# Kernel tuning notes

Measured on AMD Instinct MI355X. Metric: run time of the kernel, lower is better.

Reference implementation:

```python
import math
import jax, jax.numpy as jnp
import numpy as np

B, L = 64, 25
FEAT, HEADS, LAYERS = 128, 8, 2
USER_N, POI_N, CAT_N = 5000, 10000, 400


def _autocorr(q, k, v):
    # q,k,v: [B,L,H,E] ; training-mode AutoCorrelation (self.training=True)
    Lq = q.shape[1]
    qp = jnp.transpose(q, (0, 2, 3, 1))  # [B,H,E,L]
    kp = jnp.transpose(k, (0, 2, 3, 1))
    vp = jnp.transpose(v, (0, 2, 3, 1))
    qf = jnp.fft.rfft(qp, axis=-1)
    kf = jnp.fft.rfft(kp, axis=-1)
    corr = jnp.fft.irfft(qf * jnp.conj(kf), n=Lq, axis=-1)  # [B,H,E,L]
    top_k = int(1 * math.log(Lq))  # factor=1 -> 3 for L=25
    mean_value = corr.mean(axis=(1, 2))  # [B,L]
    _, index = jax.lax.top_k(mean_value.mean(axis=0), top_k)  # [K], shared across batch
    weights = mean_value[:, index]  # [B,K]
    tmp_corr = jax.nn.softmax(weights, axis=-1)
    # roll(values, -delay) == gather at (t + delay) mod L
    gidx = (jnp.arange(Lq)[None, :] + index[:, None]) % Lq  # [K,L]
    patterns = vp[..., gidx]  # [B,H,E,K,L]
    agg = jnp.einsum('bhekl,bk->bhel', patterns, tmp_corr)  # weighted delay aggregation
    return jnp.transpose(agg, (0, 3, 1, 2))  # [B,L,H,E]


def _ac_layer(qx, kx, vx, w, b):
    # w: [4, d, d] torch-layout [out,in] for (q,k,v,out) projections; b: [4, d]
    Bq, Lq, d = qx.shape
    q = (qx @ w[0].T + b[0]).reshape(Bq, Lq, HEADS, -1)
    k = (kx @ w[1].T + b[1]).reshape(Bq, kx.shape[1], HEADS, -1)
    v = (vx @ w[2].T + b[2]).reshape(Bq, vx.shape[1], HEADS, -1)
    out = _autocorr(q, k, v).reshape(Bq, Lq, -1)
    return out @ w[3].T + b[3]


def setup_inputs() -> dict:
    key = jax.random.key(0)
    ks = jax.random.split(key, 16)
    d = FEAT
    inp = {
        'user': jax.random.randint(ks[0], (B, L), 0, USER_N),
        'poi': jax.random.randint(ks[1], (B, L), 0, POI_N),
        'cat': jax.random.randint(ks[2], (B, L), 0, CAT_N),
        'lat': jax.random.normal(ks[3], (B, L), jnp.float32),
        'lon': jax.random.normal(ks[4], (B, L), jnp.float32),
        'tod': jax.random.randint(ks[5], (B, L), 0, 24),
        'dow': jax.random.randint(ks[6], (B, L), 0, 7),
        'unixtime': jax.random.normal(ks[7], (B, L), jnp.float32),
        'user_emb': jax.random.normal(ks[8], (USER_N, d), jnp.float32) * 0.02,
        'poi_emb': jax.random.normal(ks[9], (POI_N, d), jnp.float32) * 0.02,
        'cat_emb': jax.random.normal(ks[10], (CAT_N, d), jnp.float32) * 0.02,
        'tod_emb': jax.random.normal(ks[11], (24, d), jnp.float32) * 0.02,
        'dow_emb': jax.random.normal(ks[12], (7, d), jnp.float32) * 0.02,
        'user_embc': jax.random.normal(jax.random.fold_in(ks[8], 1), (USER_N, d), jnp.float32) * 0.02,
        'tod_embc': jax.random.normal(jax.random.fold_in(ks[11], 1), (24, d), jnp.float32) * 0.02,
        'dow_embc': jax.random.normal(jax.random.fold_in(ks[12], 1), (7, d), jnp.float32) * 0.02,
        # W[layer, module(poi,cat,xpoi,xcat), proj(q,k,v,o), out, in]
        'W': jax.random.normal(ks[13], (LAYERS, 4, 4, d, d), jnp.float32) * (1.0 / math.sqrt(d)),
        'Bv': jnp.zeros((LAYERS, 4, 4, d), jnp.float32),
        'value_w': jax.random.normal(ks[14], (1, L), jnp.float32) * 0.1,
        'value_b': jnp.zeros((1,), jnp.float32),
        'distance_matrix': jax.random.uniform(ks[15], (POI_N, POI_N), jnp.float32) * 10.0,
    }
    return inp


def reference(user, poi, cat, lat, lon, tod, dow, unixtime,
              user_emb, poi_emb, cat_emb, tod_emb, dow_emb,
              user_embc, tod_embc, dow_embc,
              W, Bv, value_w, value_b, distance_matrix):
    x = user_emb[user] + poi_emb[poi] + tod_emb[tod] + dow_emb[dow]        # [B,L,d]
    xc = user_embc[user] + cat_emb[cat] + tod_embc[tod] + dow_embc[dow]   # [B,L,d]

    interval_dis = distance_matrix[poi]  # [B,L,P] row gather == index_select loop
    interval = jnp.exp(-interval_dis / (interval_dis.max() - interval_dis.min()))

    out, outc = x, xc
    for i in range(LAYERS):
        out = _ac_layer(out, out, out, W[i, 0], Bv[i, 0])
        outc = _ac_layer(outc, outc, outc, W[i, 1], Bv[i, 1])
        out = _ac_layer(out, outc, outc, W[i, 2], Bv[i, 2])
        outc = _ac_layer(outc, out, out, W[i, 3], Bv[i, 3])

    attn = jnp.einsum('pd,bld->bpl', poi_emb, out) * jnp.transpose(interval, (0, 2, 1))
    attn_cat = jnp.einsum('cd,bld->bcl', cat_emb, outc)
    pre_poi = (attn @ value_w.T + value_b)[..., 0]      # [B,P]
    pre_cat = (attn_cat @ value_w.T + value_b)[..., 0]  # [B,C]
    return pre_poi, pre_cat
```

## Files before the change

kernel.cpp:

```cpp
#include <hip/hip_runtime.h>
#include <hip/hip_bf16.h>

#define BB 64
#define LL 25
#define DD 128
#define BL 1600
#define POI_N 10000
#define CAT_N 400

__global__ __launch_bounds__(256) void embed_kernel(
    const int* __restrict__ user, const int* __restrict__ poi, const int* __restrict__ cat,
    const int* __restrict__ tod, const int* __restrict__ dow,
    const float* __restrict__ ue, const float* __restrict__ pe, const float* __restrict__ ce,
    const float* __restrict__ te, const float* __restrict__ de,
    const float* __restrict__ uec, const float* __restrict__ tec, const float* __restrict__ dec,
    float* __restrict__ x, float* __restrict__ xc, unsigned* __restrict__ mm)
{
    int idx = blockIdx.x * 256 + threadIdx.x;
    if (idx == 0) { mm[0] = 0u; mm[1] = 0x7f7fffffu; }
    int bl = idx >> 7, d = idx & 127;
    int u = user[bl], p = poi[bl], c = cat[bl], td = tod[bl], dw = dow[bl];
    x[idx]  = ue[u * DD + d] + pe[p * DD + d] + te[td * DD + d] + de[dw * DD + d];
    xc[idx] = uec[u * DD + d] + ce[c * DD + d] + tec[td * DD + d] + dec[dw * DD + d];
}

__global__ __launch_bounds__(256) void minmax_kernel(
    const int* __restrict__ poi, const float* __restrict__ Dm, unsigned* __restrict__ mm)
{
    int bl = blockIdx.x;
    const float4* r = (const float4*)(Dm + (size_t)poi[bl] * POI_N);
    float mx = -1e30f, mn = 1e30f;
    for (int i = threadIdx.x; i < POI_N / 4; i += 256) {
        float4 v4 = r[i];
        mx = fmaxf(mx, fmaxf(fmaxf(v4.x, v4.y), fmaxf(v4.z, v4.w)));
        mn = fminf(mn, fminf(fminf(v4.x, v4.y), fminf(v4.z, v4.w)));
    }
    for (int off = 32; off > 0; off >>= 1) {
        mx = fmaxf(mx, __shfl_down(mx, off));
        mn = fminf(mn, __shfl_down(mn, off));
    }
    __shared__ float smx[4], smn[4];
    int lid = threadIdx.x & 63, wid = threadIdx.x >> 6;
    if (lid == 0) { smx[wid] = mx; smn[wid] = mn; }
    __syncthreads();
    if (threadIdx.x == 0) {
        mx = fmaxf(fmaxf(smx[0], smx[1]), fmaxf(smx[2], smx[3]));
        mn = fminf(fminf(smn[0], smn[1]), fminf(smn[2], smn[3]));
        atomicMax(&mm[0], __float_as_uint(mx));
        atomicMin(&mm[1], __float_as_uint(mn));
    }
}

__global__ __launch_bounds__(256) void proj_kernel(
    const float* __restrict__ sq, const float* __restrict__ sk, const float* __restrict__ sv,
    const float* __restrict__ Wbase, const float* __restrict__ Bbase,
    float* __restrict__ q, float* __restrict__ k, float* __restrict__ v)
{
    int r = blockIdx.y;
    const float* src = (r == 0) ? sq : (r == 1 ? sk : sv);
    float* dst       = (r == 0) ? q  : (r == 1 ? k  : v);
    const float* Wm   = Wbase + r * DD * DD;
    const float* bias = Bbase + r * DD;
    int mbase = blockIdx.x * 32;
    __shared__ float sS[32][132];
    __shared__ float sWc[128][68];
    int t = threadIdx.x;

    for (int i = t; i < 32 * 32; i += 256) {
        int m = i >> 5, c = (i & 31) << 2;
        *(float4*)&sS[m][c] = *(const float4*)(src + (mbase + m) * DD + c);
    }
    __syncthreads();

    int nh = t & 31, mg = t >> 5;
    float acc[4][4] = {};
    for (int kb = 0; kb < 128; kb += 64) {
        for (int i = t; i < 128 * 16; i += 256) {
            int n = i >> 4, c = (i & 15) << 2;
            *(float4*)&sWc[n][c] = *(const float4*)(Wm + n * DD + kb + c);
        }
        __syncthreads();
#pragma unroll 4
        for (int kk = 0; kk < 64; kk += 4) {
            float4 a[4], w[4];
#pragma unroll
            for (int i2 = 0; i2 < 4; i2++) a[i2] = *(const float4*)&sS[mg * 4 + i2][kb + kk];
#pragma unroll
            for (int j = 0; j < 4; j++) w[j] = *(const float4*)&sWc[nh + 32 * j][kk];
#pragma unroll
            for (int i2 = 0; i2 < 4; i2++)
#pragma unroll
                for (int j = 0; j < 4; j++)
                    acc[i2][j] += a[i2].x * w[j].x + a[i2].y * w[j].y +
                                  a[i2].z * w[j].z + a[i2].w * w[j].w;
        }
        __syncthreads();
    }
#pragma unroll
    for (int i2 = 0; i2 < 4; i2++) {
        int m = mbase + mg * 4 + i2;
#pragma unroll
        for (int j = 0; j < 4; j++) {
            int n = nh + 32 * j;
            dst[m * DD + n] = acc[i2][j] + bias[n];
        }
    }
}

__global__ __launch_bounds__(256) void corr_kernel(
    const float* __restrict__ q, const float* __restrict__ k, float* __restrict__ mv)
{
    int b = blockIdx.x;
    __shared__ float sq[LL * DD], sk[LL * DD];
    __shared__ float rbuf[LL][4];
    int t = threadIdx.x;
    for (int i = t; i < 800; i += 256) {
        int c = i << 2;
        *(float4*)&sq[c] = *(const float4*)(q + b * LL * DD + c);
        *(float4*)&sk[c] = *(const float4*)(k + b * LL * DD + c);
    }
    __syncthreads();
    int lid = t & 63, wid = t >> 6;
    for (int tau = 0; tau < LL; tau++) {
        float s = 0.f;
        for (int e = t; e < LL * DD; e += 256) {
            int srow = e >> 7, d = e & 127;
            int qrow = srow + tau; if (qrow >= LL) qrow -= LL;
            s += sq[qrow * DD + d] * sk[e];
        }
        for (int off = 32; off > 0; off >>= 1) s += __shfl_down(s, off);
        if (lid == 0) rbuf[tau][wid] = s;
    }
    __syncthreads();
    if (t < LL)
        mv[b * LL + t] = (rbuf[t][0] + rbuf[t][1] + rbuf[t][2] + rbuf[t][3]) * (1.0f / 128.0f);
}

__global__ void topsm_kernel(const float* __restrict__ mv, float* __restrict__ tc,
                             int* __restrict__ idxout)
{
    __shared__ float sbm[LL];
    __shared__ int sidx[3];
    int t = threadIdx.x;
    if (t < LL) {
        float s = 0.f;
        for (int b = 0; b < BB; b++) s += mv[b * LL + t];
        sbm[t] = s;
    }
    __syncthreads();
    if (t == 0) {
        float loc[LL];
        for (int i = 0; i < LL; i++) loc[i] = sbm[i];
        for (int j = 0; j < 3; j++) {
            int bi = 0; float bvv = loc[0];
            for (int i = 1; i < LL; i++) if (loc[i] > bvv) { bvv = loc[i]; bi = i; }
            sidx[j] = bi; idxout[j] = bi; loc[bi] = -1e30f;
        }
    }
    __syncthreads();
    if (t < BB) {
        float w0 = mv[t * LL + sidx[0]];
        float w1 = mv[t * LL + sidx[1]];
        float w2 = mv[t * LL + sidx[2]];
        float m = fmaxf(w0, fmaxf(w1, w2));
        float e0 = expf(w0 - m), e1 = expf(w1 - m), e2 = expf(w2 - m);
        float inv = 1.0f / (e0 + e1 + e2);
        tc[t * 4 + 0] = e0 * inv; tc[t * 4 + 1] = e1 * inv; tc[t * 4 + 2] = e2 * inv;
    }
}

__global__ __launch_bounds__(256) void aggproj_kernel(
    const float* __restrict__ v, const float* __restrict__ tc, const int* __restrict__ idx3,
    const float* __restrict__ Wm, const float* __restrict__ bias, float* __restrict__ dst)
{
    int mbase = blockIdx.x * 32;
    __shared__ float sS[32][132];
    __shared__ float sWc[128][68];
    int t = threadIdx.x;
    int i0 = idx3[0], i1 = idx3[1], i2x = idx3[2];

    for (int i = t; i < 32 * 32; i += 256) {
        int m = i >> 5, c = (i & 31) << 2;
        int row = mbase + m;
        int b = row / LL, l = row - b * LL;
        int l0 = l + i0;  if (l0 >= LL) l0 -= LL;
        int l1 = l + i1;  if (l1 >= LL) l1 -= LL;
        int l2 = l + i2x; if (l2 >= LL) l2 -= LL;
        float w0 = tc[b * 4 + 0], w1 = tc[b * 4 + 1], w2 = tc[b * 4 + 2];
        float4 v0 = *(const float4*)(v + (b * LL + l0) * DD + c);
        float4 v1 = *(const float4*)(v + (b * LL + l1) * DD + c);
        float4 v2 = *(const float4*)(v + (b * LL + l2) * DD + c);
        float4 a;
        a.x = w0 * v0.x + w1 * v1.x + w2 * v2.x;
        a.y = w0 * v0.y + w1 * v1.y + w2 * v2.y;
        a.z = w0 * v0.z + w1 * v1.z + w2 * v2.z;
        a.w = w0 * v0.w + w1 * v1.w + w2 * v2.w;
        *(float4*)&sS[m][c] = a;
    }
    __syncthreads();

    int nh = t & 31, mg = t >> 5;
    float acc[4][4] = {};
    for (int kb = 0; kb < 128; kb += 64) {
        for (int i = t; i < 128 * 16; i += 256) {
            int n = i >> 4, c = (i & 15) << 2;
            *(float4*)&sWc[n][c] = *(const float4*)(Wm + n * DD + kb + c);
        }
        __syncthreads();
#pragma unroll 4
        for (int kk = 0; kk < 64; kk += 4) {
            float4 a[4], w[4];
#pragma unroll
            for (int ii = 0; ii < 4; ii++) a[ii] = *(const float4*)&sS[mg * 4 + ii][kb + kk];
#pragma unroll
            for (int j = 0; j < 4; j++) w[j] = *(const float4*)&sWc[nh + 32 * j][kk];
#pragma unroll
            for (int ii = 0; ii < 4; ii++)
#pragma unroll
                for (int j = 0; j < 4; j++)
                    acc[ii][j] += a[ii].x * w[j].x + a[ii].y * w[j].y +
                                  a[ii].z * w[j].z + a[ii].w * w[j].w;
        }
        __syncthreads();
    }
#pragma unroll
    for (int ii = 0; ii < 4; ii++) {
        int m = mbase + mg * 4 + ii;
#pragma unroll
        for (int j = 0; j < 4; j++) {
            int n = nh + 32 * j;
            dst[m * DD + n] = acc[ii][j] + bias[n];
        }
    }
}

__global__ __launch_bounds__(256) void precat_kernel(
    const float* __restrict__ outc, const float* __restrict__ cat_emb,
    const float* __restrict__ vw, const float* __restrict__ vbp, float* __restrict__ dstc)
{
    int b = blockIdx.x, t = threadIdx.x;
    __shared__ float y[DD];
    __shared__ float svw[LL];
    if (t < LL) svw[t] = vw[t];
    __syncthreads();
    if (t < DD) {
        float s = 0.f;
        for (int l = 0; l < LL; l++) s += svw[l] * outc[(b * LL + l) * DD + t];
        y[t] = s;
    }
    __syncthreads();
    float vb = vbp[0];
    for (int c = t; c < CAT_N; c += 256) {
        float s = 0.f;
        for (int d = 0; d < DD; d += 4) {
            float4 ce4 = *(const float4*)(cat_emb + c * DD + d);
            s += ce4.x * y[d] + ce4.y * y[d + 1] + ce4.z * y[d + 2] + ce4.w * y[d + 3];
        }
        dstc[b * CAT_N + c] = s + vb;
    }
}

__global__ __launch_bounds__(256) void prepoi_kernel(
    const float* __restrict__ outp, const float* __restrict__ poi_emb,
    const int* __restrict__ poi_idx, const float* __restrict__ Dm,
    const unsigned* __restrict__ mm, const float* __restrict__ vw,
    const float* __restrict__ vbp, float* __restrict__ dstp)
{
    int b = blockIdx.y;
    int pbase = blockIdx.x << 7;
    __shared__ float sO[LL][132];
    __shared__ float sPc[128][68];
    __shared__ float sS[LL][132];
    __shared__ float svw[LL];
    __shared__ int srow[LL];
    __shared__ float red[128];
    int t = threadIdx.x;

    for (int i = t; i < 800; i += 256) {
        int l = i >> 5, c = (i & 31) << 2;
        *(float4*)&sO[l][c] = *(const float4*)(outp + (b * LL + l) * DD + c);
    }
    if (t < LL) { svw[t] = vw[t]; srow[t] = poi_idx[b * LL + t]; }
    __syncthreads();

    int nh = t & 31, mg = t >> 5;
    float acc[4][4] = {};
    for (int kb = 0; kb < 128; kb += 64) {
        for (int i = t; i < 128 * 16; i += 256) {
            int p = i >> 4, c = (i & 15) << 2;
            float4 val = {0.f, 0.f, 0.f, 0.f};
            if (pbase + p < POI_N) val = *(const float4*)(poi_emb + (pbase + p) * DD + kb + c);
            *(float4*)&sPc[p][c] = val;
        }
        __syncthreads();
#pragma unroll 4
        for (int kk = 0; kk < 64; kk += 4) {
            float4 a0 = *(const float4*)&sO[mg][kb + kk];
            float4 a1 = *(const float4*)&sO[mg + 8][kb + kk];
            float4 a2 = *(const float4*)&sO[mg + 16][kb + kk];
            float4 a3 = {0.f, 0.f, 0.f, 0.f};
            if (mg == 0) a3 = *(const float4*)&sO[24][kb + kk];
#pragma unroll
            for (int j = 0; j < 4; j++) {
                float4 p4 = *(const float4*)&sPc[nh + 32 * j][kk];
                acc[j][0] += p4.x * a0.x + p4.y * a0.y + p4.z * a0.z + p4.w * a0.w;
                acc[j][1] += p4.x * a1.x + p4.y * a1.y + p4.z * a1.z + p4.w * a1.w;
                acc[j][2] += p4.x * a2.x + p4.y * a2.y + p4.z * a2.z + p4.w * a2.w;
                acc[j][3] += p4.x * a3.x + p4.y * a3.y + p4.z * a3.z + p4.w * a3.w;
            }
        }
        __syncthreads();
    }
#pragma unroll
    for (int j = 0; j < 4; j++) {
        int pl = nh + 32 * j;
        sS[mg][pl]      = acc[j][0];
        sS[mg + 8][pl]  = acc[j][1];
        sS[mg + 16][pl] = acc[j][2];
        if (mg == 0) sS[24][pl] = acc[j][3];
    }
    __syncthreads();

    float gmax = __uint_as_float(mm[0]);
    float gmin = __uint_as_float(mm[1]);
    float ninv = -1.0f / (gmax - gmin);
    int pp = t & 127, half = t >> 7;
    int p = pbase + pp;
    float s = 0.f;
    if (p < POI_N) {
        int l0 = half ? 13 : 0, l1 = half ? 25 : 13;
        for (int l = l0; l < l1; l++) {
            float dv = Dm[(size_t)srow[l] * POI_N + p];
            s += svw[l] * expf(dv * ninv) * sS[l][pp];
        }
    }
    if (half) red[pp] = s;
    __syncthreads();
    if (!half && p < POI_N)
        dstp[(size_t)b * POI_N + p] = s + red[pp] + vbp[0];
}

extern "C" void kernel_launch(void* const* d_in, const int* in_sizes, int n_in,
                              void* d_out, int out_size, void* d_ws, size_t ws_size,
                              hipStream_t stream)
{
    const int*   user = (const int*)d_in[0];
    const int*   poi  = (const int*)d_in[1];
    const int*   cat  = (const int*)d_in[2];
    const int*   tod  = (const int*)d_in[5];
    const int*   dow  = (const int*)d_in[6];
    const float* ue   = (const float*)d_in[8];
    const float* pe   = (const float*)d_in[9];
    const float* ce   = (const float*)d_in[10];
    const float* te   = (const float*)d_in[11];
    const float* de   = (const float*)d_in[12];
    const float* uec  = (const float*)d_in[13];
    const float* tec  = (const float*)d_in[14];
    const float* dec  = (const float*)d_in[15];
    const float* W    = (const float*)d_in[16];
    const float* Bv   = (const float*)d_in[17];
    const float* vw   = (const float*)d_in[18];
    const float* vb   = (const float*)d_in[19];
    const float* Dm   = (const float*)d_in[20];

    float* ws = (float*)d_ws;
    float* O0 = ws;
    float* C0 = ws + 204800;
    float* O1 = ws + 409600;
    float* C1 = ws + 614400;
    float* Q  = ws + 819200;
    float* Kb = ws + 1024000;
    float* V  = ws + 1228800;
    float* MV = ws + 1433600;
    float* TC = ws + 1435200;
    int*   IDX = (int*)(ws + 1435456);
    unsigned* MM = (unsigned*)(ws + 1435460);

    float* out_poi = (float*)d_out;
    float* out_cat = out_poi + BB * POI_N;

    embed_kernel<<<800, 256, 0, stream>>>(user, poi, cat, tod, dow,
                                          ue, pe, ce, te, de, uec, tec, dec, O0, C0, MM);
    minmax_kernel<<<BL, 256, 0, stream>>>(poi, Dm, MM);

    auto ac = [&](const float* qx, const float* kx, const float* vx, int i, int j, float* dstbuf) {
        const float* Wb = W + (size_t)((i * 4 + j) * 4) * DD * DD;
        const float* Bb = Bv + (size_t)((i * 4 + j) * 4) * DD;
        proj_kernel<<<dim3(50, 3), 256, 0, stream>>>(qx, kx, vx, Wb, Bb, Q, Kb, V);
        corr_kernel<<<BB, 256, 0, stream>>>(Q, Kb, MV);
        topsm_kernel<<<1, 256, 0, stream>>>(MV, TC, IDX);
        aggproj_kernel<<<50, 256, 0, stream>>>(V, TC, IDX, Wb + 3 * DD * DD, Bb + 3 * DD, dstbuf);
    };

    ac(O0, O0, O0, 0, 0, O1);
    ac(C0, C0, C0, 0, 1, C1);
    ac(O1, C1, C1, 0, 2, O0);
    ac(C1, O0, O0, 0, 3, C0);
    ac(O0, O0, O0, 1, 0, O1);
    ac(C0, C0, C0, 1, 1, C1);
    ac(O1, C1, C1, 1, 2, O0);
    ac(C1, O0, O0, 1, 3, C0);

    precat_kernel<<<BB, 256, 0, stream>>>(C0, ce, vw, vb, out_cat);
    prepoi_kernel<<<dim3(79, BB), 256, 0, stream>>>(O0, pe, poi, Dm, MM, vw, vb, out_poi);
}
```

Before: 1.203 ms.

## Fuse embed, minmax, and all autocorrelation layers into one persistent kernel with grid barriers

Replaces the embed, minmax, and 32 per-layer kernel launches (projection, correlation, top-k/softmax, aggregation+projection) plus precat with a single persistent kernel of 150 blocks that synchronizes stages through atomic-counter grid barriers. Top-k/softmax is recomputed redundantly in each aggregation block instead of running as a separate single-block kernel. The min is tracked with atomicMax on the bitwise complement so a single memset can zero both counters. This removes launch overhead and inter-kernel gaps, but relies on all 150 blocks being co-resident for the spin barriers and loses the extra parallelism from splitting minmax over 1600 blocks.

```diff
diff --git a/kernel.cpp b/kernel.cpp
--- a/kernel.cpp
+++ b/kernel.cpp
@@ -1,5 +1,4 @@
 #include <hip/hip_runtime.h>
-#include <hip/hip_bf16.h>
 
 #define BB 64
 #define LL 25
@@ -7,256 +6,293 @@
 #define BL 1600
 #define POI_N 10000
 #define CAT_N 400
-
-__global__ __launch_bounds__(256) void embed_kernel(
+#define NBLK 150
+
+__device__ __forceinline__ void gridbar(unsigned* __restrict__ bar, int id)
+{
+    __syncthreads();
+    if (threadIdx.x == 0) {
+        __threadfence();
+        __hip_atomic_fetch_add(&bar[id], 1u, __ATOMIC_RELEASE, __HIP_MEMORY_SCOPE_AGENT);
+        while (__hip_atomic_load(&bar[id], __ATOMIC_ACQUIRE, __HIP_MEMORY_SCOPE_AGENT) < NBLK)
+            __builtin_amdgcn_s_sleep(1);
+    }
+    __syncthreads();
+}
+
+__global__ __launch_bounds__(256) void persist_kernel(
     const int* __restrict__ user, const int* __restrict__ poi, const int* __restrict__ cat,
     const int* __restrict__ tod, const int* __restrict__ dow,
     const float* __restrict__ ue, const float* __restrict__ pe, const float* __restrict__ ce,
     const float* __restrict__ te, const float* __restrict__ de,
     const float* __restrict__ uec, const float* __restrict__ tec, const float* __restrict__ dec,
-    float* __restrict__ x, float* __restrict__ xc, unsigned* __restrict__ mm)
+    const float* __restrict__ W, const float* __restrict__ Bv,
+    const float* __restrict__ vw, const float* __restrict__ vbp,
+    const float* __restrict__ Dm,
+    float* __restrict__ O0, float* __restrict__ C0, float* __restrict__ O1, float* __restrict__ C1,
+    float* __restrict__ Qb, float* __restrict__ Kb, float* __restrict__ Vb,
+    float* __restrict__ MV,
+    unsigned* __restrict__ bar, unsigned* __restrict__ mm,
+    float* __restrict__ out_cat)
 {
-    int idx = blockIdx.x * 256 + threadIdx.x;
-    if (idx == 0) { mm[0] = 0u; mm[1] = 0x7f7fffffu; }
-    int bl = idx >> 7, d = idx & 127;
-    int u = user[bl], p = poi[bl], c = cat[bl], td = tod[bl], dw = dow[bl];
-    x[idx]  = ue[u * DD + d] + pe[p * DD + d] + te[td * DD + d] + de[dw * DD + d];
-    xc[idx] = uec[u * DD + d] + ce[c * DD + d] + tec[td * DD + d] + dec[dw * DD + d];
-}
-
-__global__ __launch_bounds__(256) void minmax_kernel(
-    const int* __restrict__ poi, const float* __restrict__ Dm, unsigned* __restrict__ mm)
-{
-    int bl = blockIdx.x;
-    const float4* r = (const float4*)(Dm + (size_t)poi[bl] * POI_N);
-    float mx = -1e30f, mn = 1e30f;
-    for (int i = threadIdx.x; i < POI_N / 4; i += 256) {
-        float4 v4 = r[i];
-        mx = fmaxf(mx, fmaxf(fmaxf(v4.x, v4.y), fmaxf(v4.z, v4.w)));
-        mn = fminf(mn, fminf(fminf(v4.x, v4.y), fminf(v4.z, v4.w)));
-    }
-    for (int off = 32; off > 0; off >>= 1) {
-        mx = fmaxf(mx, __shfl_down(mx, off));
-        mn = fminf(mn, __shfl_down(mn, off));
-    }
-    __shared__ float smx[4], smn[4];
-    int lid = threadIdx.x & 63, wid = threadIdx.x >> 6;
-    if (lid == 0) { smx[wid] = mx; smn[wid] = mn; }
-    __syncthreads();
-    if (threadIdx.x == 0) {
-        mx = fmaxf(fmaxf(smx[0], smx[1]), fmaxf(smx[2], smx[3]));
-        mn = fminf(fminf(smn[0], smn[1]), fminf(smn[2], smn[3]));
-        atomicMax(&mm[0], __float_as_uint(mx));
-        atomicMin(&mm[1], __float_as_uint(mn));
-    }
-}
-
-__global__ __launch_bounds__(256) void proj_kernel(
-    const float* __restrict__ sq, const float* __restrict__ sk, const float* __restrict__ sv,
-    const float* __restrict__ Wbase, const float* __restrict__ Bbase,
-    float* __restrict__ q, float* __restrict__ k, float* __restrict__ v)
-{
-    int r = blockIdx.y;
-    const float* src = (r == 0) ? sq : (r == 1 ? sk : sv);
-    float* dst       = (r == 0) ? q  : (r == 1 ? k  : v);
-    const float* Wm   = Wbase + r * DD * DD;
-    const float* bias = Bbase + r * DD;
-    int mbase = blockIdx.x * 32;
-    __shared__ float sS[32][132];
-    __shared__ float sWc[128][68];
-    int t = threadIdx.x;
-
-    for (int i = t; i < 32 * 32; i += 256) {
-        int m = i >> 5, c = (i & 31) << 2;
-        *(float4*)&sS[m][c] = *(const float4*)(src + (mbase + m) * DD + c);
-    }
-    __syncthreads();
-
-    int nh = t & 31, mg = t >> 5;
-    float acc[4][4] = {};
-    for (int kb = 0; kb < 128; kb += 64) {
-        for (int i = t; i < 128 * 16; i += 256) {
-            int n = i >> 4, c = (i & 15) << 2;
-            *(float4*)&sWc[n][c] = *(const float4*)(Wm + n * DD + kb + c);
-        }
+    __shared__ __align__(16) char smem_raw[51712];
+    float (*sS)[132] = reinterpret_cast<float(*)[132]>(smem_raw);
+    float (*sWc)[68] = reinterpret_cast<float(*)[68]>(smem_raw + 16896);
+    float* csq       = reinterpret_cast<float*>(smem_raw);
+    float* csk       = reinterpret_cast<float*>(smem_raw + 12800);
+    float (*crb)[4]  = reinterpret_cast<float(*)[4]>(smem_raw + 25600);
+
+    __shared__ float sbm[LL];
+    __shared__ int   sidx[3];
+    __shared__ float stc[BB][3];
+    __shared__ float redA[4], redB[4];
+    __shared__ float yv[DD];
+    __shared__ float svw[LL];
+
+    int bx = blockIdx.x, t = threadIdx.x;
+
+    for (int i = bx * 256 + t; i < 51200; i += NBLK * 256) {
+        int bl = i >> 5, c = (i & 31) << 2;
+        int u = user[bl], p = poi[bl], cc = cat[bl], td = tod[bl], dw = dow[bl];
+        float4 a0 = *(const float4*)(ue + u * DD + c);
+        float4 a1 = *(const float4*)(pe + p * DD + c);
+        float4 a2 = *(const float4*)(te + td * DD + c);
+        float4 a3 = *(const float4*)(de + dw * DD + c);
+        float4 x;
+        x.x = a0.x + a1.x + a2.x + a3.x; x.y = a0.y + a1.y + a2.y + a3.y;
+        x.z = a0.z + a1.z + a2.z + a3.z; x.w = a0.w + a1.w + a2.w + a3.w;
+        *(float4*)(O0 + bl * DD + c) = x;
+        float4 b0 = *(const float4*)(uec + u * DD + c);
+        float4 b1 = *(const float4*)(ce + cc * DD + c);
+        float4 b2 = *(const float4*)(tec + td * DD + c);
+        float4 b3 = *(const float4*)(dec + dw * DD + c);
+        float4 xc;
+        xc.x = b0.x + b1.x + b2.x + b3.x; xc.y = b0.y + b1.y + b2.y + b3.y;
+        xc.z = b0.z + b1.z + b2.z + b3.z; xc.w = b0.w + b1.w + b2.w + b3.w;
+        *(float4*)(C0 + bl * DD + c) = xc;
+    }
+    {
+        float mx = -1e30f, mn = 1e30f;
+        for (int row = bx; row < BL; row += NBLK) {
+            const float4* r4 = (const float4*)(Dm + (size_t)poi[row] * POI_N);
+            for (int i = t; i < POI_N / 4; i += 256) {
+                float4 v4 = r4[i];
+                mx = fmaxf(mx, fmaxf(fmaxf(v4.x, v4.y), fmaxf(v4.z, v4.w)));
+                mn = fminf(mn, fminf(fminf(v4.x, v4.y), fminf(v4.z, v4.w)));
+            }
+        }
+        for (int off = 32; off > 0; off >>= 1) {
+            mx = fmaxf(mx, __shfl_down(mx, off));
+            mn = fminf(mn, __shfl_down(mn, off));
+        }
+        if ((t & 63) == 0) { redA[t >> 6] = mx; redB[t >> 6] = mn; }
         __syncthreads();
+        if (t == 0) {
+            mx = fmaxf(fmaxf(redA[0], redA[1]), fmaxf(redA[2], redA[3]));
+            mn = fminf(fminf(redB[0], redB[1]), fminf(redB[2], redB[3]));
+            atomicMax(&mm[0], __float_as_uint(mx));
+            atomicMax(&mm[1], ~__float_as_uint(mn));
+        }
+    }
+    gridbar(bar, 0);
+
+    float* bufs[4] = {O0, C0, O1, C1};
+    const int qsel[8] = {0, 1, 2, 3, 0, 1, 2, 3};
+    const int ksel[8] = {0, 1, 3, 0, 0, 1, 3, 0};
+    const int dsel[8] = {2, 3, 0, 1, 2, 3, 0, 1};
+    int bid = 1;
+
+#pragma unroll 1
+    for (int ci = 0; ci < 8; ++ci) {
+        const float* qx  = bufs[qsel[ci]];
+        const float* kx  = bufs[ksel[ci]];
+        float*       dst = bufs[dsel[ci]];
+        const float* Wb  = W  + (size_t)ci * 4 * DD * DD;
+        const float* Bb  = Bv + (size_t)ci * 4 * DD;
+
+        {
+            int r = bx / 50, tile = bx % 50;
+            const float* src  = (r == 0) ? qx : kx;
+            const float* Wm   = Wb + r * DD * DD;
+            const float* bias = Bb + r * DD;
+            float* pdst       = (r == 0) ? Qb : (r == 1 ? Kb : Vb);
+            int mbase = tile * 32;
+
+            for (int i = t; i < 32 * 32; i += 256) {
+                int m = i >> 5, c = (i & 31) << 2;
+                *(float4*)&sS[m][c] = *(const float4*)(src + (mbase + m) * DD + c);
+            }
+            __syncthreads();
+            int nh = t & 31, mg = t >> 5;
+            float acc[4][4] = {};
+            for (int kb = 0; kb < 128; kb += 64) {
+                for (int i = t; i < 128 * 16; i += 256) {
+                    int n = i >> 4, c = (i & 15) << 2;
+                    *(float4*)&sWc[n][c] = *(const float4*)(Wm + n * DD + kb + c);
+                }
+                __syncthreads();
 #pragma unroll 4
-        for (int kk = 0; kk < 64; kk += 4) {
-            float4 a[4], w[4];
-#pragma unroll
-            for (int i2 = 0; i2 < 4; i2++) a[i2] = *(const float4*)&sS[mg * 4 + i2][kb + kk];
-#pragma unroll
-            for (int j = 0; j < 4; j++) w[j] = *(const float4*)&sWc[nh + 32 * j][kk];
-#pragma unroll
-            for (int i2 = 0; i2 < 4; i2++)
-#pragma unroll
-                for (int j = 0; j < 4; j++)
-                    acc[i2][j] += a[i2].x * w[j].x + a[i2].y * w[j].y +
-                                  a[i2].z * w[j].z + a[i2].w * w[j].w;
-        }
+                for (int kk = 0; kk < 64; kk += 4) {
+                    float4 a[4], w[4];
+#pragma unroll
+                    for (int i2 = 0; i2 < 4; i2++) a[i2] = *(const float4*)&sS[mg * 4 + i2][kb + kk];
+#pragma unroll
+                    for (int j = 0; j < 4; j++) w[j] = *(const float4*)&sWc[nh + 32 * j][kk];
+#pragma unroll
+                    for (int i2 = 0; i2 < 4; i2++)
+#pragma unroll
+                        for (int j = 0; j < 4; j++)
+                            acc[i2][j] += a[i2].x * w[j].x + a[i2].y * w[j].y +
+                                          a[i2].z * w[j].z + a[i2].w * w[j].w;
+                }
+                __syncthreads();
+            }
+#pragma unroll
+            for (int i2 = 0; i2 < 4; i2++) {
+                int m = mbase + mg * 4 + i2;
+#pragma unroll
+                for (int j = 0; j < 4; j++) {
+                    int n = nh + 32 * j;
+                    pdst[m * DD + n] = acc[i2][j] + bias[n];
+                }
+            }
+        }
+        gridbar(bar, bid++);
+
+        if (bx < BB) {
+            int b = bx;
+            for (int i = t; i < 800; i += 256) {
+                int c = i << 2;
+                *(float4*)&csq[c] = *(const float4*)(Qb + b * LL * DD + c);
+                *(float4*)&csk[c] = *(const float4*)(Kb + b * LL * DD + c);
+            }
+            __syncthreads();
+            int lid = t & 63, wid = t >> 6;
+            for (int tau = 0; tau < LL; tau++) {
+                float s = 0.f;
+                for (int e = t; e < 800; e += 256) {
+                    int srow = e >> 5, dc = (e & 31) << 2;
+                    int qrow = srow + tau; if (qrow >= LL) qrow -= LL;
+                    float4 a = *(const float4*)&csq[qrow * DD + dc];
+                    float4 g = *(const float4*)&csk[srow * DD + dc];
+                    s += a.x * g.x + a.y * g.y + a.z * g.z + a.w * g.w;
+                }
+                for (int off = 32; off > 0; off >>= 1) s += __shfl_down(s, off);
+                if (lid == 0) crb[tau][wid] = s;
+            }
+            __syncthreads();
+            if (t < LL)
+                MV[b * LL + t] = (crb[t][0] + crb[t][1] + crb[t][2] + crb[t][3]) * (1.0f / 128.0f);
+        }
+        gridbar(bar, bid++);
+
+        if (bx < 50) {
+            int mbase = bx * 32;
+            if (t < LL) {
+                float s = 0.f;
+                for (int b2 = 0; b2 < BB; b2++) s += MV[b2 * LL + t];
+                sbm[t] = s;
+            }
+            __syncthreads();
+            if (t == 0) {
+                float loc[LL];
+                for (int i = 0; i < LL; i++) loc[i] = sbm[i];
+                for (int j = 0; j < 3; j++) {
+                    int bi = 0; float bvv = loc[0];
+                    for (int i = 1; i < LL; i++) if (loc[i] > bvv) { bvv = loc[i]; bi = i; }
+                    sidx[j] = bi; loc[bi] = -1e30f;
+                }
+            }
+            __syncthreads();
+            if (t < BB) {
+                float w0 = MV[t * LL + sidx[0]];
+                float w1 = MV[t * LL + sidx[1]];
+                float w2 = MV[t * LL + sidx[2]];
+                float m = fmaxf(w0, fmaxf(w1, w2));
+                float e0 = expf(w0 - m), e1 = expf(w1 - m), e2 = expf(w2 - m);
+                float inv = 1.0f / (e0 + e1 + e2);
+                stc[t][0] = e0 * inv; stc[t][1] = e1 * inv; stc[t][2] = e2 * inv;
+            }
+            __syncthreads();
+            int i0 = sidx[0], i1 = sidx[1], i2x = sidx[2];
+            const float* Wm   = Wb + 3 * DD * DD;
+            const float* bias = Bb + 3 * DD;
+
+            for (int i = t; i < 32 * 32; i += 256) {
+                int m = i >> 5, c = (i & 31) << 2;
+                int row = mbase + m;
+                int b = row / LL, l = row - b * LL;
+                int l0 = l + i0;  if (l0 >= LL) l0 -= LL;
+                int l1 = l + i1;  if (l1 >= LL) l1 -= LL;
+                int l2 = l + i2x; if (l2 >= LL) l2 -= LL;
+                float w0 = stc[b][0], w1 = stc[b][1], w2 = stc[b][2];
+                float4 v0 = *(const float4*)(Vb + (b * LL + l0) * DD + c);
+                float4 v1 = *(const float4*)(Vb + (b * LL + l1) * DD + c);
+                float4 v2 = *(const float4*)(Vb + (b * LL + l2) * DD + c);
+                float4 a;
+                a.x = w0 * v0.x + w1 * v1.x + w2 * v2.x;
+                a.y = w0 * v0.y + w1 * v1.y + w2 * v2.y;
+                a.z = w0 * v0.z + w1 * v1.z + w2 * v2.z;
+                a.w = w0 * v0.w + w1 * v1.w + w2 * v2.w;
+                *(float4*)&sS[m][c] = a;
+            }
+            __syncthreads();
+            int nh = t & 31, mg = t >> 5;
+            float acc[4][4] = {};
+            for (int kb = 0; kb < 128; kb += 64) {
+                for (int i = t; i < 128 * 16; i += 256) {
+                    int n = i >> 4, c = (i & 15) << 2;
+                    *(float4*)&sWc[n][c] = *(const float4*)(Wm + n * DD + kb + c);
+                }
+                __syncthreads();
+#pragma unroll 4
+                for (int kk = 0; kk < 64; kk += 4) {
+                    float4 a[4], w[4];
+#pragma unroll
+                    for (int ii = 0; ii < 4; ii++) a[ii] = *(const float4*)&sS[mg * 4 + ii][kb + kk];
+#pragma unroll
+                    for (int j = 0; j < 4; j++) w[j] = *(const float4*)&sWc[nh + 32 * j][kk];
+#pragma unroll
+                    for (int ii = 0; ii < 4; ii++)
+#pragma unroll
+                        for (int j = 0; j < 4; j++)
+                            acc[ii][j] += a[ii].x * w[j].x + a[ii].y * w[j].y +
+                                          a[ii].z * w[j].z + a[ii].w * w[j].w;
+                }
+                __syncthreads();
+            }
+#pragma unroll
+            for (int ii = 0; ii < 4; ii++) {
+                int m = mbase + mg * 4 + ii;
+#pragma unroll
+                for (int j = 0; j < 4; j++) {
+                    int n = nh + 32 * j;
+                    dst[m * DD + n] = acc[ii][j] + bias[n];
+                }
+            }
+        }
+        gridbar(bar, bid++);
+    }
+
+    if (bx < BB) {
+        int b = bx;
+        if (t < LL) svw[t] = vw[t];
         __syncthreads();
-    }
-#pragma unroll
-    for (int i2 = 0; i2 < 4; i2++) {
-        int m = mbase + mg * 4 + i2;
-#pragma unroll
-        for (int j = 0; j < 4; j++) {
-            int n = nh + 32 * j;
-            dst[m * DD + n] = acc[i2][j] + bias[n];
-        }
-    }
-}
-
-__global__ __launch_bounds__(256) void corr_kernel(
-    const float* __restrict__ q, const float* __restrict__ k, float* __restrict__ mv)
-{
-    int b = blockIdx.x;
-    __shared__ float sq[LL * DD], sk[LL * DD];
-    __shared__ float rbuf[LL][4];
-    int t = threadIdx.x;
-    for (int i = t; i < 800; i += 256) {
-        int c = i << 2;
-        *(float4*)&sq[c] = *(const float4*)(q + b * LL * DD + c);
-        *(float4*)&sk[c] = *(const float4*)(k + b * LL * DD + c);
-    }
-    __syncthreads();
-    int lid = t & 63, wid = t >> 6;
-    for (int tau = 0; tau < LL; tau++) {
-        float s = 0.f;
-        for (int e = t; e < LL * DD; e += 256) {
-            int srow = e >> 7, d = e & 127;
-            int qrow = srow + tau; if (qrow >= LL) qrow -= LL;
-            s += sq[qrow * DD + d] * sk[e];
-        }
-        for (int off = 32; off > 0; off >>= 1) s += __shfl_down(s, off);
-        if (lid == 0) rbuf[tau][wid] = s;
-    }
-    __syncthreads();
-    if (t < LL)
-        mv[b * LL + t] = (rbuf[t][0] + rbuf[t][1] + rbuf[t][2] + rbuf[t][3]) * (1.0f / 128.0f);
-}
-
-__global__ void topsm_kernel(const float* __restrict__ mv, float* __restrict__ tc,
-                             int* __restrict__ idxout)
-{
-    __shared__ float sbm[LL];
-    __shared__ int sidx[3];
-    int t = threadIdx.x;
-    if (t < LL) {
-        float s = 0.f;
-        for (int b = 0; b < BB; b++) s += mv[b * LL + t];
-        sbm[t] = s;
-    }
-    __syncthreads();
-    if (t == 0) {
-        float loc[LL];
-        for (int i = 0; i < LL; i++) loc[i] = sbm[i];
-        for (int j = 0; j < 3; j++) {
-            int bi = 0; float bvv = loc[0];
-            for (int i = 1; i < LL; i++) if (loc[i] > bvv) { bvv = loc[i]; bi = i; }
-            sidx[j] = bi; idxout[j] = bi; loc[bi] = -1e30f;
-        }
-    }
-    __syncthreads();
-    if (t < BB) {
-        float w0 = mv[t * LL + sidx[0]];
-        float w1 = mv[t * LL + sidx[1]];
-        float w2 = mv[t * LL + sidx[2]];
-        float m = fmaxf(w0, fmaxf(w1, w2));
-        float e0 = expf(w0 - m), e1 = expf(w1 - m), e2 = expf(w2 - m);
-        float inv = 1.0f / (e0 + e1 + e2);
-        tc[t * 4 + 0] = e0 * inv; tc[t * 4 + 1] = e1 * inv; tc[t * 4 + 2] = e2 * inv;
-    }
-}
-
-__global__ __launch_bounds__(256) void aggproj_kernel(
-    const float* __restrict__ v, const float* __restrict__ tc, const int* __restrict__ idx3,
-    const float* __restrict__ Wm, const float* __restrict__ bias, float* __restrict__ dst)
-{
-    int mbase = blockIdx.x * 32;
-    __shared__ float sS[32][132];
-    __shared__ float sWc[128][68];
-    int t = threadIdx.x;
-    int i0 = idx3[0], i1 = idx3[1], i2x = idx3[2];
-
-    for (int i = t; i < 32 * 32; i += 256) {
-        int m = i >> 5, c = (i & 31) << 2;
-        int row = mbase + m;
-        int b = row / LL, l = row - b * LL;
-        int l0 = l + i0;  if (l0 >= LL) l0 -= LL;
-        int l1 = l + i1;  if (l1 >= LL) l1 -= LL;
-        int l2 = l + i2x; if (l2 >= LL) l2 -= LL;
-        float w0 = tc[b * 4 + 0], w1 = tc[b * 4 + 1], w2 = tc[b * 4 + 2];
-        float4 v0 = *(const float4*)(v + (b * LL + l0) * DD + c);
-        float4 v1 = *(const float4*)(v + (b * LL + l1) * DD + c);
-        float4 v2 = *(const float4*)(v + (b * LL + l2) * DD + c);
-        float4 a;
-        a.x = w0 * v0.x + w1 * v1.x + w2 * v2.x;
-        a.y = w0 * v0.y + w1 * v1.y + w2 * v2.y;
-        a.z = w0 * v0.z + w1 * v1.z + w2 * v2.z;
-        a.w = w0 * v0.w + w1 * v1.w + w2 * v2.w;
-        *(float4*)&sS[m][c] = a;
-    }
-    __syncthreads();
-
-    int nh = t & 31, mg = t >> 5;
-    float acc[4][4] = {};
-    for (int kb = 0; kb < 128; kb += 64) {
-        for (int i = t; i < 128 * 16; i += 256) {
-            int n = i >> 4, c = (i & 15) << 2;
-            *(float4*)&sWc[n][c] = *(const float4*)(Wm + n * DD + kb + c);
+        if (t < DD) {
+            float s = 0.f;
+            for (int l = 0; l < LL; l++) s += svw[l] * C0[(b * LL + l) * DD + t];
+            yv[t] = s;
         }
         __syncthreads();
-#pragma unroll 4
-        for (int kk = 0; kk < 64; kk += 4) {
-            float4 a[4], w[4];
-#pragma unroll
-            for (int ii = 0; ii < 4; ii++) a[ii] = *(const float4*)&sS[mg * 4 + ii][kb + kk];
-#pragma unroll
-            for (int j = 0; j < 4; j++) w[j] = *(const float4*)&sWc[nh + 32 * j][kk];
-#pragma unroll
-            for (int ii = 0; ii < 4; ii++)
-#pragma unroll
-                for (int j = 0; j < 4; j++)
-                    acc[ii][j] += a[ii].x * w[j].x + a[ii].y * w[j].y +
-                                  a[ii].z * w[j].z + a[ii].w * w[j].w;
-        }
-        __syncthreads();
-    }
-#pragma unroll
-    for (int ii = 0; ii < 4; ii++) {
-        int m = mbase + mg * 4 + ii;
-#pragma unroll
-        for (int j = 0; j < 4; j++) {
-            int n = nh + 32 * j;
-            dst[m * DD + n] = acc[ii][j] + bias[n];
-        }
-    }
-}
-
-__global__ __launch_bounds__(256) void precat_kernel(
-    const float* __restrict__ outc, const float* __restrict__ cat_emb,
-    const float* __restrict__ vw, const float* __restrict__ vbp, float* __restrict__ dstc)
-{
-    int b = blockIdx.x, t = threadIdx.x;
-    __shared__ float y[DD];
-    __shared__ float svw[LL];
-    if (t < LL) svw[t] = vw[t];
-    __syncthreads();
-    if (t < DD) {
-        float s = 0.f;
-        for (int l = 0; l < LL; l++) s += svw[l] * outc[(b * LL + l) * DD + t];
-        y[t] = s;
-    }
-    __syncthreads();
-    float vb = vbp[0];
-    for (int c = t; c < CAT_N; c += 256) {
-        float s = 0.f;
-        for (int d = 0; d < DD; d += 4) {
-            float4 ce4 = *(const float4*)(cat_emb + c * DD + d);
-            s += ce4.x * y[d] + ce4.y * y[d + 1] + ce4.z * y[d + 2] + ce4.w * y[d + 3];
-        }
-        dstc[b * CAT_N + c] = s + vb;
+        float vb = vbp[0];
+        for (int c = t; c < CAT_N; c += 256) {
+            float s = 0.f;
+            for (int d = 0; d < DD; d += 4) {
+                float4 ce4 = *(const float4*)(ce + c * DD + d);
+                s += ce4.x * yv[d] + ce4.y * yv[d + 1] + ce4.z * yv[d + 2] + ce4.w * yv[d + 3];
+            }
+            out_cat[b * CAT_N + c] = s + vb;
+        }
     }
 }
 
@@ -322,7 +358,7 @@
     __syncthreads();
 
     float gmax = __uint_as_float(mm[0]);
-    float gmin = __uint_as_float(mm[1]);
+    float gmin = __uint_as_float(~mm[1]);
     float ninv = -1.0f / (gmax - gmin);
     int pp = t & 127, half = t >> 7;
     int p = pbase + pp;
@@ -372,35 +408,17 @@
     float* Kb = ws + 1024000;
     float* V  = ws + 1228800;
     float* MV = ws + 1433600;
-    float* TC = ws + 1435200;
-    int*   IDX = (int*)(ws + 1435456);
-    unsigned* MM = (unsigned*)(ws + 1435460);
+    unsigned* BAR = (unsigned*)(ws + 1435200);
+    unsigned* MM  = BAR + 32;
 
     float* out_poi = (float*)d_out;
     float* out_cat = out_poi + BB * POI_N;
 
-    embed_kernel<<<800, 256, 0, stream>>>(user, poi, cat, tod, dow,
-                                          ue, pe, ce, te, de, uec, tec, dec, O0, C0, MM);
-    minmax_kernel<<<BL, 256, 0, stream>>>(poi, Dm, MM);
-
-    auto ac = [&](const float* qx, const float* kx, const float* vx, int i, int j, float* dstbuf) {
-        const float* Wb = W + (size_t)((i * 4 + j) * 4) * DD * DD;
-        const float* Bb = Bv + (size_t)((i * 4 + j) * 4) * DD;
-        proj_kernel<<<dim3(50, 3), 256, 0, stream>>>(qx, kx, vx, Wb, Bb, Q, Kb, V);
-        corr_kernel<<<BB, 256, 0, stream>>>(Q, Kb, MV);
-        topsm_kernel<<<1, 256, 0, stream>>>(MV, TC, IDX);
-        aggproj_kernel<<<50, 256, 0, stream>>>(V, TC, IDX, Wb + 3 * DD * DD, Bb + 3 * DD, dstbuf);
-    };
-
-    ac(O0, O0, O0, 0, 0, O1);
-    ac(C0, C0, C0, 0, 1, C1);
-    ac(O1, C1, C1, 0, 2, O0);
-    ac(C1, O0, O0, 0, 3, C0);
-    ac(O0, O0, O0, 1, 0, O1);
-    ac(C0, C0, C0, 1, 1, C1);
-    ac(O1, C1, C1, 1, 2, O0);
-    ac(C1, O0, O0, 1, 3, C0);
-
-    precat_kernel<<<BB, 256, 0, stream>>>(C0, ce, vw, vb, out_cat);
+    hipMemsetAsync(BAR, 0, 34 * sizeof(unsigned), stream);
+
+    persist_kernel<<<NBLK, 256, 0, stream>>>(
+        user, poi, cat, tod, dow, ue, pe, ce, te, de, uec, tec, dec,
+        W, Bv, vw, vb, Dm, O0, C0, O1, C1, Q, Kb, V, MV, BAR, MM, out_cat);
+
     prepoi_kernel<<<dim3(79, BB), 256, 0, stream>>>(O0, pe, poi, Dm, MM, vw, vb, out_poi);
 }
```

Measured after the change: 1.362 ms. 13.2% more time.
